# Kernel tuning notes

Hardware: AMD Instinct MI355X
Metric: run time of the kernel (lower is better)

## Reference

```python
import jax, jax.numpy as jnp
import numpy as np

NR_OF_BINS = 64
F_MIN = -4.0
F_MAX = 4.0


def setup_inputs() -> dict:
    key = jax.random.key(0)
    x = jax.random.normal(key, (32, 512, 1024), dtype=jnp.float32)
    # tf.linspace(fMin, fMax, nr_of_bins - 1) -> Discretization boundaries
    boundaries = jnp.linspace(F_MIN, F_MAX, NR_OF_BINS - 1, dtype=jnp.float32)
    return {"x": x, "boundaries": boundaries, "nr_of_bins": NR_OF_BINS}


def reference(x, boundaries, nr_of_bins):
    # x: (B, T, F). TF Discretization / Bucketize: bin = #boundaries <= x,
    # which is searchsorted(boundaries, x, side='right').
    B, T, F = x.shape
    bins = jnp.searchsorted(boundaries, x, side="right")  # (B, T, F) int32 in [0, nr_of_bins)
    # Single-pass histogram over the feature axis via scatter-add instead of
    # the original nr_of_bins-pass equality+reduce loop.
    row_ids = jnp.arange(B * T, dtype=bins.dtype)[:, None]  # (B*T, 1)
    flat_idx = (row_ids * nr_of_bins + bins.reshape(B * T, F)).reshape(-1)
    counts = jnp.zeros((B * T * nr_of_bins,), dtype=jnp.float32).at[flat_idx].add(1.0)
    counts = counts.reshape(B, T, nr_of_bins)
    # Normalize each histogram to sum to 1 (divide by per-row total = F).
    z = counts / jnp.sum(counts, axis=2, keepdims=True)
    return z
```

## Files before the change

kernel.cpp:

```cpp
#include <hip/hip_runtime.h>

#define FDIM 1024
#define NBINS 64
#define NB 63
#define WAVES_PER_BLOCK 4
#define SUBHIST 4

__global__ __launch_bounds__(256) void dist_tok_kernel(
    const float* __restrict__ x, const float* __restrict__ bnd,
    float* __restrict__ out, int nrows)
{
    __shared__ float s_bnd[NB];
    __shared__ unsigned int s_hist[WAVES_PER_BLOCK][SUBHIST][NBINS];

    const int tid  = threadIdx.x;
    const int wave = tid >> 6;
    const int lane = tid & 63;
    const int grp  = lane >> 4;

    if (tid < NB) s_bnd[tid] = bnd[tid];

    #pragma unroll
    for (int i = 0; i < SUBHIST; ++i)
        s_hist[wave][i][lane] = 0u;

    __syncthreads();

    const int row = blockIdx.x * WAVES_PER_BLOCK + wave;
    if (row < nrows) {
        const float4* xr = (const float4*)(x + (size_t)row * FDIM);
        const float inv_h = 62.0f / 8.0f;
        #pragma unroll
        for (int c = 0; c < 4; ++c) {
            float4 v = xr[c * 64 + lane];
            float vals[4] = {v.x, v.y, v.z, v.w};
            #pragma unroll
            for (int e = 0; e < 4; ++e) {
                float xv = vals[e];
                int j = (int)floorf((xv + 4.0f) * inv_h) + 1;
                j = j < 0 ? 0 : (j > NB ? NB : j);
                while (j < NB && s_bnd[j] <= xv) ++j;
                while (j > 0 && s_bnd[j - 1] > xv) --j;
                atomicAdd(&s_hist[wave][grp][j], 1u);
            }
        }
    }

    __syncthreads();

    if (row < nrows) {
        unsigned int total = s_hist[wave][0][lane] + s_hist[wave][1][lane]
                           + s_hist[wave][2][lane] + s_hist[wave][3][lane];
        out[(size_t)row * NBINS + lane] = (float)total * (1.0f / (float)FDIM);
    }
}

extern "C" void kernel_launch(void* const* d_in, const int* in_sizes, int n_in,
                              void* d_out, int out_size, void* d_ws, size_t ws_size,
                              hipStream_t stream) {
    const float* x   = (const float*)d_in[0];
    const float* bnd = (const float*)d_in[1];
    float* out = (float*)d_out;

    const int nrows = in_sizes[0] / FDIM;
    const int grid  = (nrows + WAVES_PER_BLOCK - 1) / WAVES_PER_BLOCK;

    dist_tok_kernel<<<grid, 256, 0, stream>>>(x, bnd, out, nrows);
}
```

Baseline: 21.73 us.

## Pad boundaries with sentinels, hoist row loads, and swizzle sub-histogram bins

Pads the shared boundary table with -inf/+inf sentinels so bin lookup needs one fma-based guess and a two-value check, with a rarely taken correction loop. All four float4 loads for the row are issued up front instead of one per iteration. Each lane group's sub-histogram index is XOR-swizzled so the groups land on different LDS banks, and the final reduction un-swizzles it. The aim is to cut branching in the search and LDS bank conflicts on the atomics, at the cost of holding more registers.

```diff
diff --git a/kernel.cpp b/kernel.cpp
--- a/kernel.cpp
+++ b/kernel.cpp
@@ -1,4 +1,5 @@
 #include <hip/hip_runtime.h>
+#include <math.h>
 
 #define FDIM 1024
 #define NBINS 64
@@ -10,15 +11,17 @@
     const float* __restrict__ x, const float* __restrict__ bnd,
     float* __restrict__ out, int nrows)
 {
-    __shared__ float s_bnd[NB];
+    __shared__ float s_bndp[NB + 2];
     __shared__ unsigned int s_hist[WAVES_PER_BLOCK][SUBHIST][NBINS];
 
     const int tid  = threadIdx.x;
     const int wave = tid >> 6;
     const int lane = tid & 63;
     const int grp  = lane >> 4;
+    const int gx   = grp << 3;
 
-    if (tid < NB) s_bnd[tid] = bnd[tid];
+    if (tid < NB) s_bndp[tid + 1] = bnd[tid];
+    if (tid == NB) { s_bndp[0] = -INFINITY; s_bndp[NB + 1] = INFINITY; }
 
     #pragma unroll
     for (int i = 0; i < SUBHIST; ++i)
@@ -29,28 +32,35 @@
     const int row = blockIdx.x * WAVES_PER_BLOCK + wave;
     if (row < nrows) {
         const float4* xr = (const float4*)(x + (size_t)row * FDIM);
-        const float inv_h = 62.0f / 8.0f;
+        float4 v0 = xr[lane];
+        float4 v1 = xr[64 + lane];
+        float4 v2 = xr[128 + lane];
+        float4 v3 = xr[192 + lane];
+
+        float vals[16] = {v0.x, v0.y, v0.z, v0.w, v1.x, v1.y, v1.z, v1.w,
+                          v2.x, v2.y, v2.z, v2.w, v3.x, v3.y, v3.z, v3.w};
         #pragma unroll
-        for (int c = 0; c < 4; ++c) {
-            float4 v = xr[c * 64 + lane];
-            float vals[4] = {v.x, v.y, v.z, v.w};
-            #pragma unroll
-            for (int e = 0; e < 4; ++e) {
-                float xv = vals[e];
-                int j = (int)floorf((xv + 4.0f) * inv_h) + 1;
-                j = j < 0 ? 0 : (j > NB ? NB : j);
-                while (j < NB && s_bnd[j] <= xv) ++j;
-                while (j > 0 && s_bnd[j - 1] > xv) --j;
-                atomicAdd(&s_hist[wave][grp][j], 1u);
+        for (int e = 0; e < 16; ++e) {
+            float xv = vals[e];
+            int j = (int)fmaf(xv, 7.75f, 32.0f);
+            j = j < 0 ? 0 : (j > NB ? NB : j);
+            float lo = s_bndp[j];
+            float hi = s_bndp[j + 1];
+            if (__builtin_expect(!(lo <= xv && xv < hi), 0)) {
+                while (s_bndp[j + 1] <= xv) ++j;
+                while (s_bndp[j] > xv) --j;
             }
+            atomicAdd(&s_hist[wave][grp][j ^ gx], 1u);
         }
     }
 
     __syncthreads();
 
     if (row < nrows) {
-        unsigned int total = s_hist[wave][0][lane] + s_hist[wave][1][lane]
-                           + s_hist[wave][2][lane] + s_hist[wave][3][lane];
+        unsigned int total = s_hist[wave][0][lane]
+                           + s_hist[wave][1][lane ^ 8]
+                           + s_hist[wave][2][lane ^ 16]
+                           + s_hist[wave][3][lane ^ 24];
         out[(size_t)row * NBINS + lane] = (float)total * (1.0f / (float)FDIM);
     }
 }
```

Result: faster. 17.86 us (-17.8%).
